# Kernel optimization log

Hardware: AMD Instinct MI355X
Metric: run time of the kernel (lower is better)

The kernel has to match this reference:

```python
import jax, jax.numpy as jnp
import numpy as np

N = 100000   # num_nodes
E = 1250000  # num_edges
IN = 64
HID = 64
OUT = 64
LN_EPS = 1e-5


def _gcn_conv(x, src, dst, W, b, n):
    # PyG GCNConv: add self-loops, symmetric deg^{-1/2} normalization, then linear.
    h = x @ W  # (N, out)
    deg = jax.ops.segment_sum(jnp.ones(src.shape[0], h.dtype), dst, num_segments=n) + 1.0  # +1 self-loop
    dinv = jax.lax.rsqrt(deg)
    norm = dinv[src] * dinv[dst]  # (E,)
    out = jax.ops.segment_sum(h[src] * norm[:, None], dst, num_segments=n)
    out = out + h * (dinv * dinv)[:, None]  # self-loop message
    return out + b


def _sage_conv(x, src, dst, Wl, bl, Wr, n):
    # PyG SAGEConv(aggr='mean'): lin_l(mean_{j in N(i)} x_j) + lin_r(x_i); bias only in lin_l.
    cnt = jax.ops.segment_sum(jnp.ones(src.shape[0], x.dtype), dst, num_segments=n)
    agg = jax.ops.segment_sum(x[src], dst, num_segments=n) / jnp.maximum(cnt, 1.0)[:, None]
    return agg @ Wl + bl + x @ Wr


def _layer_norm(x, g, b):
    mu = jnp.mean(x, axis=-1, keepdims=True)
    var = jnp.var(x, axis=-1, keepdims=True)
    return (x - mu) * jax.lax.rsqrt(var + LN_EPS) * g + b


def setup_inputs() -> dict:
    key = jax.random.key(0)
    ks = jax.random.split(key, 16)
    def w(k, shape):
        fan_in = shape[0]
        return (jax.random.normal(k, shape, jnp.float32) / np.sqrt(fan_in)).astype(jnp.float32)
    x = jax.random.normal(ks[0], (N, IN), jnp.float32)
    edge_index = jax.random.randint(ks[1], (2, E), 0, N, dtype=jnp.int64)
    return {
        "x": x,
        "edge_index": edge_index,
        "gcn_w1": w(ks[2], (IN, HID)), "gcn_b1": jnp.zeros((HID,), jnp.float32),
        "gcn_w2": w(ks[3], (HID, OUT)), "gcn_b2": jnp.zeros((OUT,), jnp.float32),
        "sage_wl1": w(ks[4], (IN, HID)), "sage_bl1": jnp.zeros((HID,), jnp.float32),
        "sage_wr1": w(ks[5], (IN, HID)),
        "sage_wl2": w(ks[6], (HID, OUT)), "sage_bl2": jnp.zeros((OUT,), jnp.float32),
        "sage_wr2": w(ks[7], (HID, OUT)),
        "gcn_ln_g": jnp.ones((OUT,), jnp.float32), "gcn_ln_b": jnp.zeros((OUT,), jnp.float32),
        "sage_ln_g": jnp.ones((OUT,), jnp.float32), "sage_ln_b": jnp.zeros((OUT,), jnp.float32),
        "proj_w": w(ks[8], (2 * OUT, OUT)), "proj_b": jnp.zeros((OUT,), jnp.float32),
    }


def reference(x, edge_index, gcn_w1, gcn_b1, gcn_w2, gcn_b2,
              sage_wl1, sage_bl1, sage_wr1, sage_wl2, sage_bl2, sage_wr2,
              gcn_ln_g, gcn_ln_b, sage_ln_g, sage_ln_b, proj_w, proj_b):
    src, dst = edge_index[0], edge_index[1]
    n = x.shape[0]
    # GCN branch (dropout p=0 / eval -> identity)
    g = jax.nn.relu(_gcn_conv(x, src, dst, gcn_w1, gcn_b1, n))
    g = _gcn_conv(g, src, dst, gcn_w2, gcn_b2, n)
    # SAGE branch
    s = jax.nn.relu(_sage_conv(x, src, dst, sage_wl1, sage_bl1, sage_wr1, n))
    s = _sage_conv(s, src, dst, sage_wl2, sage_bl2, sage_wr2, n)
    # Norm + projected-concat fusion
    g = _layer_norm(g, gcn_ln_g, gcn_ln_b)
    s = _layer_norm(s, sage_ln_g, sage_ln_b)
    cat = jnp.concatenate([g, s], axis=-1)  # (N, 2*OUT)
    return cat @ proj_w + proj_b
```

## Files before the change

### kernel.cpp

```cpp
#include <hip/hip_runtime.h>


#define SCAN_CHUNK 2048

typedef __attribute__((ext_vector_type(8))) short short8;
typedef __attribute__((ext_vector_type(4))) short short4v;
typedef __attribute__((ext_vector_type(4))) float floatx4;

__device__ __forceinline__ unsigned short f2bf(float f) {
    unsigned int u = __float_as_uint(f);
    unsigned int r = u + 0x7FFFu + ((u >> 16) & 1u);
    return (unsigned short)(r >> 16);
}
__device__ __forceinline__ float bf2f(unsigned short h) {
    return __uint_as_float(((unsigned int)h) << 16);
}

__device__ __forceinline__ unsigned lds_addr(const void* p) {
    return (unsigned)(unsigned long long)(__attribute__((address_space(3))) const char*)p;
}

__device__ __forceinline__ void gload_lds16(const void* g, void* l) {
    __builtin_amdgcn_global_load_lds(
        (const __attribute__((address_space(1))) unsigned int*)g,
        (__attribute__((address_space(3))) unsigned int*)l, 16, 0, 0);
}

template<int NN>
__device__ __forceinline__ void wait_vmcnt() {
    if constexpr (NN == 8)      asm volatile("s_waitcnt vmcnt(8)" ::: "memory");
    else if constexpr (NN == 4) asm volatile("s_waitcnt vmcnt(4)" ::: "memory");
    else                        asm volatile("s_waitcnt vmcnt(0)" ::: "memory");
}

__device__ __forceinline__ short8 cat44(short4v lo, short4v hi) {
    short8 r;
    r[0] = lo[0]; r[1] = lo[1]; r[2] = lo[2]; r[3] = lo[3];
    r[4] = hi[0]; r[5] = hi[1]; r[6] = hi[2]; r[7] = hi[3];
    return r;
}

template<int NF, int CTB>
__device__ __forceinline__ void tr_read4(unsigned a0, short8 bf[4]) {
    short4v l0, h0, l1, h1, l2, h2, l3, h3;
    asm volatile(
        "ds_read_b64_tr_b16 %0, %8 offset:%9\n\t"
        "ds_read_b64_tr_b16 %1, %8 offset:%10\n\t"
        "ds_read_b64_tr_b16 %2, %8 offset:%11\n\t"
        "ds_read_b64_tr_b16 %3, %8 offset:%12\n\t"
        "ds_read_b64_tr_b16 %4, %8 offset:%13\n\t"
        "ds_read_b64_tr_b16 %5, %8 offset:%14\n\t"
        "ds_read_b64_tr_b16 %6, %8 offset:%15\n\t"
        "ds_read_b64_tr_b16 %7, %8 offset:%16\n\t"
        "s_waitcnt lgkmcnt(0)"
        : "=&v"(l0), "=&v"(h0), "=&v"(l1), "=&v"(h1),
          "=&v"(l2), "=&v"(h2), "=&v"(l3), "=&v"(h3)
        : "v"(a0),
          "i"((0 * NF + CTB + 0) * 128), "i"((1 * NF + CTB + 0) * 128),
          "i"((0 * NF + CTB + 1) * 128), "i"((1 * NF + CTB + 1) * 128),
          "i"((0 * NF + CTB + 2) * 128), "i"((1 * NF + CTB + 2) * 128),
          "i"((0 * NF + CTB + 3) * 128), "i"((1 * NF + CTB + 3) * 128)
        : "memory");
    bf[0] = cat44(l0, h0);
    bf[1] = cat44(l1, h1);
    bf[2] = cat44(l2, h2);
    bf[3] = cat44(l3, h3);
}

__global__ void k_count(const int* __restrict__ ei, int E, int* __restrict__ cnt,
                        int* __restrict__ rank) {
    int i = blockIdx.x * blockDim.x + threadIdx.x;
    int e = i * 4;
    if (e + 4 <= E) {
        int4 d = *(const int4*)&ei[E + e];
        int4 r;
        r.x = atomicAdd(&cnt[d.x], 1);
        r.y = atomicAdd(&cnt[d.y], 1);
        r.z = atomicAdd(&cnt[d.z], 1);
        r.w = atomicAdd(&cnt[d.w], 1);
        *(int4*)&rank[e] = r;
    } else {
        for (int j = e; j < E; ++j) rank[j] = atomicAdd(&cnt[ei[E + j]], 1);
    }
}

__global__ void k_scan_reduce(const int* __restrict__ cnt, int N, int* __restrict__ blockSums) {
    __shared__ int lds[256];
    int base = blockIdx.x * SCAN_CHUNK;
    int t = threadIdx.x;
    int s = 0;
    for (int j = 0; j < 8; ++j) {
        int idx = base + t * 8 + j;
        if (idx < N) s += cnt[idx] + 1;
    }
    lds[t] = s;
    __syncthreads();
    for (int d = 128; d > 0; d >>= 1) {
        if (t < d) lds[t] += lds[t + d];
        __syncthreads();
    }
    if (t == 0) blockSums[blockIdx.x] = lds[0];
}

__global__ void k_scan_spine(int* __restrict__ blockSums, int B) {
    if (threadIdx.x == 0 && blockIdx.x == 0) {
        int run = 0;
        for (int b = 0; b < B; ++b) { int v = blockSums[b]; blockSums[b] = run; run += v; }
    }
}

__global__ void k_scan_write(const int* __restrict__ cnt, int N,
                             const int* __restrict__ blockSums,
                             int* __restrict__ offs, float* __restrict__ dinv) {
    __shared__ int lds[256];
    int base = blockIdx.x * SCAN_CHUNK;
    int t = threadIdx.x;
    int v[8];
    int s = 0;
    for (int j = 0; j < 8; ++j) {
        int idx = base + t * 8 + j;
        v[j] = (idx < N) ? cnt[idx] : 0;
        s += (idx < N) ? v[j] + 1 : 0;
    }
    lds[t] = s;
    __syncthreads();
    for (int d = 1; d < 256; d <<= 1) {
        int x = (t >= d) ? lds[t - d] : 0;
        __syncthreads();
        lds[t] += x;
        __syncthreads();
    }
    int excl = (t == 0) ? 0 : lds[t - 1];
    int run = blockSums[blockIdx.x] + excl;
    for (int j = 0; j < 8; ++j) {
        int idx = base + t * 8 + j;
        if (idx < N) {
            offs[idx] = run;
            run += v[j] + 1;
            dinv[idx] = rsqrtf((float)v[j] + 1.0f);
            if (idx == N - 1) offs[N] = run;
        }
    }
}

__global__ void k_fill(const int* __restrict__ ei, int E, const int* __restrict__ offs,
                       const int* __restrict__ rank, const float* __restrict__ dinv,
                       int* __restrict__ csr, unsigned int* __restrict__ pk, int use_pk) {
    int i = blockIdx.x * blockDim.x + threadIdx.x;
    int e = i * 4;
    if (e + 4 <= E) {
        int4 s = *(const int4*)&ei[e];
        int4 d = *(const int4*)&ei[E + e];
        int4 r = *(const int4*)&rank[e];
        int p0 = offs[d.x] + r.x, p1 = offs[d.y] + r.y;
        int p2 = offs[d.z] + r.z, p3 = offs[d.w] + r.w;
        csr[p0] = s.x; csr[p1] = s.y; csr[p2] = s.z; csr[p3] = s.w;
        if (use_pk) {
            pk[p0] = ((unsigned)(d.x & 15) << 16) | f2bf(dinv[s.x] * dinv[d.x]);
            pk[p1] = ((unsigned)(d.y & 15) << 16) | f2bf(dinv[s.y] * dinv[d.y]);
            pk[p2] = ((unsigned)(d.z & 15) << 16) | f2bf(dinv[s.z] * dinv[d.z]);
            pk[p3] = ((unsigned)(d.w & 15) << 16) | f2bf(dinv[s.w] * dinv[d.w]);
        }
    } else {
        for (int j = e; j < E; ++j) {
            int dd = ei[E + j];
            int p = offs[dd] + rank[j];
            csr[p] = ei[j];
            if (use_pk) pk[p] = ((unsigned)(dd & 15) << 16) | f2bf(dinv[ei[j]] * dinv[dd]);
        }
    }
}

__global__ void k_self(const int* __restrict__ offs, const int* __restrict__ cnt,
                       const float* __restrict__ dinv,
                       int* __restrict__ csr, unsigned int* __restrict__ pk, int N) {
    int i = blockIdx.x * blockDim.x + threadIdx.x;
    if (i < N) {
        int pos = offs[i] + cnt[i];
        float di = dinv[i];
        csr[pos] = i;
        pk[pos] = ((unsigned)(i & 15) << 16) | (1u << 20) | f2bf(di * di);
    }
}

__global__ void k_xtobf16(const float* __restrict__ x, unsigned short* __restrict__ xb, int total) {
    int i = blockIdx.x * blockDim.x + threadIdx.x;
    int e = i * 8;
    if (e + 8 <= total) {
        float4 a = *(const float4*)&x[e];
        float4 b = *(const float4*)&x[e + 4];
        short8 o;
        o[0] = (short)f2bf(a.x); o[1] = (short)f2bf(a.y);
        o[2] = (short)f2bf(a.z); o[3] = (short)f2bf(a.w);
        o[4] = (short)f2bf(b.x); o[5] = (short)f2bf(b.y);
        o[6] = (short)f2bf(b.z); o[7] = (short)f2bf(b.w);
        *(short8*)&xb[e] = o;
    } else {
        for (int j = e; j < total; ++j) xb[j] = f2bf(x[j]);
    }
}

template<int ROWSH>
__launch_bounds__(128)
__global__ void k_gatherM(const unsigned short* __restrict__ feat,
                          const int* __restrict__ csr,
                          const unsigned int* __restrict__ pk,
                          const int* __restrict__ offs, const int* __restrict__ cnt,
                          unsigned short* __restrict__ agg, int N) {
    constexpr int NF = ROWSH / 16;
    constexpr int LPR = ROWSH / 8;
    constexpr int EPP = 64 / LPR;
    constexpr int PASSES = 32 / EPP;

    __shared__ unsigned short sbuf[2][2][32 * ROWSH];

    const int lane = threadIdx.x & 63;
    const int wv = threadIdx.x >> 6;
    const int base = blockIdx.x * 32 + wv * 16;
    if (base >= N) return;

    const int q = lane >> 4;
    const int d16 = lane & 15;

    const int parity = lane & 1;
    const int ei_low = (lane >> 1) & 3;
    const int sf_sub = (lane >> 3) & (NF - 1);
    const int ei_high = (NF == 8) ? 0 : (lane >> 5);
    const int eid = ei_high * 4 + ei_low;
    const int sf = sf_sub * 16 + parity * 8;

    const int elo = offs[base];
    const int ehi = offs[min(base + 16, N)];
    const int emax = ehi - 1;
    const int nch = (ehi - elo + 31) >> 5;

    int cM0, cM1, cM2, cM3;
    unsigned pM0, pM1, pM2, pM3;
    {
        int i0 = elo + lane;
        int i1 = i0 + 64, i2 = i0 + 128, i3 = i0 + 192;
        cM0 = csr[i0 <= emax ? i0 : emax];
        cM1 = csr[i1 <= emax ? i1 : emax];
        cM2 = csr[i2 <= emax ? i2 : emax];
        cM3 = csr[i3 <= emax ? i3 : emax];
        unsigned t0 = pk[i0 <= emax ? i0 : emax];
        unsigned t1 = pk[i1 <= emax ? i1 : emax];
        unsigned t2 = pk[i2 <= emax ? i2 : emax];
        unsigned t3 = pk[i3 <= emax ? i3 : emax];
        pM0 = (i0 < ehi) ? t0 : 0x00100000u;
        pM1 = (i1 < ehi) ? t1 : 0x00100000u;
        pM2 = (i2 < ehi) ? t2 : 0x00100000u;
        pM3 = (i3 < ehi) ? t3 : 0x00100000u;
    }

    floatx4 accg[4], accs[4];
#pragma unroll
    for (int i = 0; i < 4; ++i) {
        accg[i] = floatx4{0.f, 0.f, 0.f, 0.f};
        accs[i] = floatx4{0.f, 0.f, 0.f, 0.f};
    }

    unsigned short* wb0 = &sbuf[wv][0][0];
    unsigned short* wb1 = &sbuf[wv][1][0];
    const unsigned a0base = (unsigned)(q * 2 * NF) * 128u + (unsigned)d16 * 8u;
    const unsigned a0_0 = lds_addr(wb0) + a0base;
    const unsigned a0_1 = lds_addr(wb1) + a0base;

    auto getmeta = [&](int c, int& cv, unsigned& pv, int& wofs) {
        int rc = c >> 1;
        if (rc < 4) {
            wofs = (c & 1) << 5;
            cv = (rc == 0) ? cM0 : (rc == 1) ? cM1 : (rc == 2) ? cM2 : cM3;
            pv = (rc == 0) ? pM0 : (rc == 1) ? pM1 : (rc == 2) ? pM2 : pM3;
        } else {
            int idx = elo + (c << 5) + lane;
            int idc = idx <= emax ? idx : emax;
            cv = csr[idc];
            unsigned t = pk[idc];
            pv = (idx < ehi) ? t : 0x00100000u;
            wofs = 0;
        }
    };

    auto issue = [&](unsigned short* dst, int cv, int wofs) {
#pragma unroll
        for (int p = 0; p < PASSES; ++p) {
            int src = __shfl(cv, wofs + p * EPP + eid, 64);
            gload_lds16(&feat[(size_t)src * ROWSH + sf], dst + p * 512);
        }
        __builtin_amdgcn_sched_barrier(0);
    };

    int cv; unsigned pv; int wofs;
    getmeta(0, cv, pv, wofs);
    issue(wb0, cv, wofs);
    unsigned pvC = pv; int wofsC = wofs;

    int cur = 0;
    for (int c = 0; c < nch; ++c) {
        bool pf = (c + 1 < nch);
        if (pf) {
            getmeta(c + 1, cv, pv, wofs);
            issue(cur ? wb0 : wb1, cv, wofs);
        }
        short8 aG, aS;
#pragma unroll
        for (int j = 0; j < 8; ++j) {
            unsigned u = (unsigned)__shfl((int)pvC, wofsC + q * 8 + j, 64);
            unsigned hi = u >> 16;
            bool match = (int)(hi & 15u) == d16;
            aG[j] = match ? (short)(u & 0xFFFFu) : (short)0;
            aS[j] = (match && !(hi & 16u)) ? (short)0x3F80 : (short)0;
        }
        if (pf) wait_vmcnt<PASSES>();
        else    wait_vmcnt<0>();
        __builtin_amdgcn_sched_barrier(0);

        const unsigned a0 = cur ? a0_1 : a0_0;
        short8 bG[4];
        tr_read4<NF, 0>(a0, bG);
#pragma unroll
        for (int ct = 0; ct < 4; ++ct)
            accg[ct] = __builtin_amdgcn_mfma_f32_16x16x32_bf16(aG, bG[ct], accg[ct], 0, 0, 0);
        if constexpr (NF == 8) {
            short8 bS[4];
            tr_read4<NF, 4>(a0, bS);
#pragma unroll
            for (int ct = 0; ct < 4; ++ct)
                accs[ct] = __builtin_amdgcn_mfma_f32_16x16x32_bf16(aS, bS[ct], accs[ct], 0, 0, 0);
        } else {
#pragma unroll
            for (int ct = 0; ct < 4; ++ct)
                accs[ct] = __builtin_amdgcn_mfma_f32_16x16x32_bf16(aS, bG[ct], accs[ct], 0, 0, 0);
        }
        pvC = pv; wofsC = wofs;
        cur ^= 1;
    }

#pragma unroll
    for (int r = 0; r < 4; ++r) {
        int node = base + q * 4 + r;
        if (node < N) {
            float rn = 1.0f / fmaxf((float)cnt[node], 1.0f);
#pragma unroll
            for (int ct = 0; ct < 4; ++ct) {
                agg[(size_t)node * 128 + ct * 16 + d16]      = f2bf(accg[ct][r]);
                agg[(size_t)node * 128 + 64 + ct * 16 + d16] = f2bf(accs[ct][r] * rn);
            }
        }
    }
}

__device__ __forceinline__ void xor_reduce8(float4& a, float4& b) {
    a.x += __shfl_xor(a.x, 16, 64); a.y += __shfl_xor(a.y, 16, 64);
    a.z += __shfl_xor(a.z, 16, 64); a.w += __shfl_xor(a.w, 16, 64);
    b.x += __shfl_xor(b.x, 16, 64); b.y += __shfl_xor(b.y, 16, 64);
    b.z += __shfl_xor(b.z, 16, 64); b.w += __shfl_xor(b.w, 16, 64);
    a.x += __shfl_xor(a.x, 32, 64); a.y += __shfl_xor(a.y, 32, 64);
    a.z += __shfl_xor(a.z, 32, 64); a.w += __shfl_xor(a.w, 32, 64);
    b.x += __shfl_xor(b.x, 32, 64); b.y += __shfl_xor(b.y, 32, 64);
    b.z += __shfl_xor(b.z, 32, 64); b.w += __shfl_xor(b.w, 32, 64);
}

__device__ __forceinline__ float red16(float v) {
    v += __shfl_xor(v, 1, 64);
    v += __shfl_xor(v, 2, 64);
    v += __shfl_xor(v, 4, 64);
    v += __shfl_xor(v, 8, 64);
    return v;
}

__global__ void k_gather1_f32(const float* __restrict__ x, const int* __restrict__ csr,
                              const int* __restrict__ offs, const int* __restrict__ cnt,
                              const float* __restrict__ dinv,
                              unsigned short* __restrict__ agg, int N) {
    int lane = threadIdx.x & 63;
    int wave = threadIdx.x >> 6;
    int node = blockIdx.x * 4 + wave;
    if (node >= N) return;
    int c = lane & 15, grp = lane >> 4;

    int st = offs[node];
    int cn = cnt[node];
    float di = dinv[node];

    float4 aA = {0.f, 0.f, 0.f, 0.f}, aB = {0.f, 0.f, 0.f, 0.f};
    for (int e = 0; e < cn; e += 8) {
        int i0 = e + grp, i1 = e + 4 + grp;
        float m0 = (i0 < cn) ? 1.f : 0.f;
        float m1 = (i1 < cn) ? 1.f : 0.f;
        int s0 = csr[st + (i0 < cn ? i0 : cn - 1)];
        int s1 = csr[st + (i1 < cn ? i1 : cn - 1)];
        float w0 = m0 * dinv[s0];
        float w1 = m1 * dinv[s1];
        float4 v0 = *(const float4*)&x[(size_t)s0 * 64 + 4 * c];
        float4 v1 = *(const float4*)&x[(size_t)s1 * 64 + 4 * c];
        aA.x += w0 * v0.x + w1 * v1.x; aA.y += w0 * v0.y + w1 * v1.y;
        aA.z += w0 * v0.z + w1 * v1.z; aA.w += w0 * v0.w + w1 * v1.w;
        aB.x += m0 * v0.x + m1 * v1.x; aB.y += m0 * v0.y + m1 * v1.y;
        aB.z += m0 * v0.z + m1 * v1.z; aB.w += m0 * v0.w + m1 * v1.w;
    }
    xor_reduce8(aA, aB);

    if (grp == 0) {
        float4 sq = *(const float4*)&x[(size_t)node * 64 + 4 * c];
        float d2 = di * di;
        ushort4 o;
        o.x = f2bf(di * aA.x + d2 * sq.x); o.y = f2bf(di * aA.y + d2 * sq.y);
        o.z = f2bf(di * aA.z + d2 * sq.z); o.w = f2bf(di * aA.w + d2 * sq.w);
        *(ushort4*)&agg[(size_t)node * 128 + 4 * c] = o;
    } else if (grp == 1) {
        float rn = 1.0f / fmaxf((float)cn, 1.0f);
        ushort4 o;
        o.x = f2bf(aB.x * rn); o.y = f2bf(aB.y * rn);
        o.z = f2bf(aB.z * rn); o.w = f2bf(aB.w * rn);
        *(ushort4*)&agg[(size_t)node * 128 + 64 + 4 * c] = o;
    }
}

__global__ void k_gather2(const unsigned short* __restrict__ gs, const int* __restrict__ csr,
                          const int* __restrict__ offs, const int* __restrict__ cnt,
                          const float* __restrict__ dinv,
                          unsigned short* __restrict__ agg, int N) {
    int lane = threadIdx.x & 63;
    int wave = threadIdx.x >> 6;
    int node = blockIdx.x * 4 + wave;
    if (node >= N) return;
    int c = lane & 15, grp = lane >> 4;

    int st = offs[node];
    int cn = cnt[node];
    float di = dinv[node];

    float4 aC = {0.f, 0.f, 0.f, 0.f}, aD = {0.f, 0.f, 0.f, 0.f};
    for (int e = 0; e < cn; e += 8) {
        int i0 = e + grp, i1 = e + 4 + grp;
        float m0 = (i0 < cn) ? 1.f : 0.f;
        float m1 = (i1 < cn) ? 1.f : 0.f;
        int s0 = csr[st + (i0 < cn ? i0 : cn - 1)];
        int s1 = csr[st + (i1 < cn ? i1 : cn - 1)];
        float w0 = m0 * dinv[s0];
        float w1 = m1 * dinv[s1];
        const unsigned short* p0 = gs + (size_t)s0 * 128 + 4 * c;
        const unsigned short* p1 = gs + (size_t)s1 * 128 + 4 * c;
        ushort4 g0u = *(const ushort4*)p0;
        ushort4 g1u = *(const ushort4*)p1;
        ushort4 t0u = *(const ushort4*)(p0 + 64);
        ushort4 t1u = *(const ushort4*)(p1 + 64);
        aC.x += w0 * bf2f(g0u.x) + w1 * bf2f(g1u.x);
        aC.y += w0 * bf2f(g0u.y) + w1 * bf2f(g1u.y);
        aC.z += w0 * bf2f(g0u.z) + w1 * bf2f(g1u.z);
        aC.w += w0 * bf2f(g0u.w) + w1 * bf2f(g1u.w);
        aD.x += m0 * bf2f(t0u.x) + m1 * bf2f(t1u.x);
        aD.y += m0 * bf2f(t0u.y) + m1 * bf2f(t1u.y);
        aD.z += m0 * bf2f(t0u.z) + m1 * bf2f(t1u.z);
        aD.w += m0 * bf2f(t0u.w) + m1 * bf2f(t1u.w);
    }
    xor_reduce8(aC, aD);

    if (grp == 0) {
        ushort4 su = *(const ushort4*)&gs[(size_t)node * 128 + 4 * c];
        float d2 = di * di;
        ushort4 o;
        o.x = f2bf(di * aC.x + d2 * bf2f(su.x));
        o.y = f2bf(di * aC.y + d2 * bf2f(su.y));
        o.z = f2bf(di * aC.z + d2 * bf2f(su.z));
        o.w = f2bf(di * aC.w + d2 * bf2f(su.w));
        *(ushort4*)&agg[(size_t)node * 128 + 4 * c] = o;
    } else if (grp == 1) {
        float rn = 1.0f / fmaxf((float)cn, 1.0f);
        ushort4 o;
        o.x = f2bf(aD.x * rn); o.y = f2bf(aD.y * rn);
        o.z = f2bf(aD.z * rn); o.w = f2bf(aD.w * rn);
        *(ushort4*)&agg[(size_t)node * 128 + 64 + 4 * c] = o;
    }
}

__launch_bounds__(512, 1)
__global__ void k_gemm1(const unsigned short* __restrict__ agg,
                        const unsigned short* __restrict__ xb,
                        const float* __restrict__ xf, int use_xb,
                        const float* __restrict__ W1, const float* __restrict__ b1,
                        const float* __restrict__ Wl1, const float* __restrict__ bl1,
                        const float* __restrict__ Wr1,
                        unsigned short* __restrict__ buf1, int N) {
    alignas(16) __shared__ unsigned short sW[3][4096];
    int t = threadIdx.x;
    for (int i = t; i < 1536; i += 512) {
        int m = i >> 9;
        int rem = i & 511;
        int f = rem >> 6;
        int L = rem & 63;
        int kb = (f >> 2) * 32 + (L >> 4) * 8;
        int o = (f & 3) * 16 + (L & 15);
        const float* Wsrc = (m == 0) ? W1 : (m == 1) ? Wl1 : Wr1;
        unsigned short* dst = &sW[m][f * 512 + L * 8];
        #pragma unroll
        for (int j = 0; j < 8; ++j) dst[j] = f2bf(Wsrc[(kb + j) * 64 + o]);
    }
    __syncthreads();

    int lane = t & 63;
    int wave = t >> 6;
    int quad = lane >> 4;
    int n16 = lane & 15;
    int base = blockIdx.x * 128 + wave * 16;
    if (base >= N) return;

    int nm = base + n16;
    if (nm >= N) nm = N - 1;
    const unsigned short* ar = agg + (size_t)nm * 128;

    {
        short8 a0 = *(const short8*)(ar + quad * 8);
        short8 a1 = *(const short8*)(ar + 32 + quad * 8);
        floatx4 g0 = {0.f, 0.f, 0.f, 0.f}, g1 = g0, g2 = g0, g3 = g0;
        g0 = __builtin_amdgcn_mfma_f32_16x16x32_bf16(a0, *(const short8*)&sW[0][0 * 512 + lane * 8], g0, 0, 0, 0);
        g0 = __builtin_amdgcn_mfma_f32_16x16x32_bf16(a1, *(const short8*)&sW[0][4 * 512 + lane * 8], g0, 0, 0, 0);
        g1 = __builtin_amdgcn_mfma_f32_16x16x32_bf16(a0, *(const short8*)&sW[0][1 * 512 + lane * 8], g1, 0, 0, 0);
        g1 = __builtin_amdgcn_mfma_f32_16x16x32_bf16(a1, *(const short8*)&sW[0][5 * 512 + lane * 8], g1, 0, 0, 0);
        g2 = __builtin_amdgcn_mfma_f32_16x16x32_bf16(a0, *(const short8*)&sW[0][2 * 512 + lane * 8], g2, 0, 0, 0);
        g2 = __builtin_amdgcn_mfma_f32_16x16x32_bf16(a1, *(const short8*)&sW[0][6 * 512 + lane * 8], g2, 0, 0, 0);
        g3 = __builtin_amdgcn_mfma_f32_16x16x32_bf16(a0, *(const short8*)&sW[0][3 * 512 + lane * 8], g3, 0, 0, 0);
        g3 = __builtin_amdgcn_mfma_f32_16x16x32_bf16(a1, *(const short8*)&sW[0][7 * 512 + lane * 8], g3, 0, 0, 0);
        floatx4 gt[4] = {g0, g1, g2, g3};
        #pragma unroll
        for (int nt = 0; nt < 4; ++nt) {
            float bg = b1[nt * 16 + n16];
            #pragma unroll
            for (int r = 0; r < 4; ++r) {
                int node = base + quad * 4 + r;
                if (node < N)
                    buf1[(size_t)node * 128 + nt * 16 + n16] = f2bf(fmaxf(gt[nt][r] + bg, 0.f));
            }
        }
    }

    {
        short8 a0 = *(const short8*)(ar + 64 + quad * 8);
        short8 a1 = *(const short8*)(ar + 96 + quad * 8);
        short8 ax0, ax1;
        if (use_xb) {
            ax0 = *(const short8*)&xb[(size_t)nm * 64 + quad * 8];
            ax1 = *(const short8*)&xb[(size_t)nm * 64 + 32 + quad * 8];
        } else {
            float4 xq0 = *(const float4*)&xf[(size_t)nm * 64 + quad * 8];
            float4 xq1 = *(const float4*)&xf[(size_t)nm * 64 + quad * 8 + 4];
            float4 xq2 = *(const float4*)&xf[(size_t)nm * 64 + 32 + quad * 8];
            float4 xq3 = *(const float4*)&xf[(size_t)nm * 64 + 32 + quad * 8 + 4];
            ax0[0] = (short)f2bf(xq0.x); ax0[1] = (short)f2bf(xq0.y);
            ax0[2] = (short)f2bf(xq0.z); ax0[3] = (short)f2bf(xq0.w);
            ax0[4] = (short)f2bf(xq1.x); ax0[5] = (short)f2bf(xq1.y);
            ax0[6] = (short)f2bf(xq1.z); ax0[7] = (short)f2bf(xq1.w);
            ax1[0] = (short)f2bf(xq2.x); ax1[1] = (short)f2bf(xq2.y);
            ax1[2] = (short)f2bf(xq2.z); ax1[3] = (short)f2bf(xq2.w);
            ax1[4] = (short)f2bf(xq3.x); ax1[5] = (short)f2bf(xq3.y);
            ax1[6] = (short)f2bf(xq3.z); ax1[7] = (short)f2bf(xq3.w);
        }

        floatx4 s0 = {0.f, 0.f, 0.f, 0.f}, s1 = s0, s2 = s0, s3 = s0;
        s0 = __builtin_amdgcn_mfma_f32_16x16x32_bf16(a0, *(const short8*)&sW[1][0 * 512 + lane * 8], s0, 0, 0, 0);
        s0 = __builtin_amdgcn_mfma_f32_16x16x32_bf16(a1, *(const short8*)&sW[1][4 * 512 + lane * 8], s0, 0, 0, 0);
        s0 = __builtin_amdgcn_mfma_f32_16x16x32_bf16(ax0, *(const short8*)&sW[2][0 * 512 + lane * 8], s0, 0, 0, 0);
        s0 = __builtin_amdgcn_mfma_f32_16x16x32_bf16(ax1, *(const short8*)&sW[2][4 * 512 + lane * 8], s0, 0, 0, 0);
        s1 = __builtin_amdgcn_mfma_f32_16x16x32_bf16(a0, *(const short8*)&sW[1][1 * 512 + lane * 8], s1, 0, 0, 0);
        s1 = __builtin_amdgcn_mfma_f32_16x16x32_bf16(a1, *(const short8*)&sW[1][5 * 512 + lane * 8], s1, 0, 0, 0);
        s1 = __builtin_amdgcn_mfma_f32_16x16x32_bf16(ax0, *(const short8*)&sW[2][1 * 512 + lane * 8], s1, 0, 0, 0);
        s1 = __builtin_amdgcn_mfma_f32_16x16x32_bf16(ax1, *(const short8*)&sW[2][5 * 512 + lane * 8], s1, 0, 0, 0);
        s2 = __builtin_amdgcn_mfma_f32_16x16x32_bf16(a0, *(const short8*)&sW[1][2 * 512 + lane * 8], s2, 0, 0, 0);
        s2 = __builtin_amdgcn_mfma_f32_16x16x32_bf16(a1, *(const short8*)&sW[1][6 * 512 + lane * 8], s2, 0, 0, 0);
        s2 = __builtin_amdgcn_mfma_f32_16x16x32_bf16(ax0, *(const short8*)&sW[2][2 * 512 + lane * 8], s2, 0, 0, 0);
        s2 = __builtin_amdgcn_mfma_f32_16x16x32_bf16(ax1, *(const short8*)&sW[2][6 * 512 + lane * 8], s2, 0, 0, 0);
        s3 = __builtin_amdgcn_mfma_f32_16x16x32_bf16(a0, *(const short8*)&sW[1][3 * 512 + lane * 8], s3, 0, 0, 0);
        s3 = __builtin_amdgcn_mfma_f32_16x16x32_bf16(a1, *(const short8*)&sW[1][7 * 512 + lane * 8], s3, 0, 0, 0);
        s3 = __builtin_amdgcn_mfma_f32_16x16x32_bf16(ax0, *(const short8*)&sW[2][3 * 512 + lane * 8], s3, 0, 0, 0);
        s3 = __builtin_amdgcn_mfma_f32_16x16x32_bf16(ax1, *(const short8*)&sW[2][7 * 512 + lane * 8], s3, 0, 0, 0);
        floatx4 stl[4] = {s0, s1, s2, s3};
        #pragma unroll
        for (int nt = 0; nt < 4; ++nt) {
            float bs = bl1[nt * 16 + n16];
            #pragma unroll
            for (int r = 0; r < 4; ++r) {
                int node = base + quad * 4 + r;
                if (node < N)
                    buf1[(size_t)node * 128 + 64 + nt * 16 + n16] = f2bf(fmaxf(stl[nt][r] + bs, 0.f));
            }
        }
    }
}

__launch_bounds__(512, 1)
__global__ void k_gemm2(const unsigned short* __restrict__ agg,
                        const unsigned short* __restrict__ buf1,
                        const float* __restrict__ W2, const float* __restrict__ b2,
                        const float* __restrict__ Wl2, const float* __restrict__ bl2,
                        const float* __restrict__ Wr2,
                        const float* __restrict__ lngG, const float* __restrict__ lnbG,
                        const float* __restrict__ lngS, const float* __restrict__ lnbS,
                        const float* __restrict__ Pw, const float* __restrict__ Pb,
                        float* __restrict__ out, int N) {
    alignas(16) __shared__ unsigned short sW[3][4096];
    alignas(16) __shared__ unsigned short sP[8192];
    alignas(16) __shared__ unsigned short sT[8][16 * 132];
    int t = threadIdx.x;
    for (int i = t; i < 1536; i += 512) {
        int m = i >> 9;
        int rem = i & 511;
        int f = rem >> 6;
        int L = rem & 63;
        int kb = (f >> 2) * 32 + (L >> 4) * 8;
        int o = (f & 3) * 16 + (L & 15);
        const float* Wsrc = (m == 0) ? W2 : (m == 1) ? Wl2 : Wr2;
        unsigned short* dst = &sW[m][f * 512 + L * 8];
        #pragma unroll
        for (int j = 0; j < 8; ++j) dst[j] = f2bf(Wsrc[(kb + j) * 64 + o]);
    }
    for (int i = t; i < 1024; i += 512) {
        int f = i >> 6;
        int L = i & 63;
        int kb = (f >> 2) * 32 + (L >> 4) * 8;
        int o = (f & 3) * 16 + (L & 15);
        unsigned short* dst = &sP[f * 512 + L * 8];
        #pragma unroll
        for (int j = 0; j < 8; ++j) dst[j] = f2bf(Pw[(kb + j) * 64 + o]);
    }
    __syncthreads();

    int lane = t & 63;
    int wave = t >> 6;
    int quad = lane >> 4;
    int n16 = lane & 15;
    int base = blockIdx.x * 128 + wave * 16;
    if (base >= N) return;
    int nm = base + n16;
    if (nm >= N) nm = N - 1;
    const unsigned short* ar = agg + (size_t)nm * 128;
    const unsigned short* br = buf1 + (size_t)nm * 128;
    unsigned short* tw = &sT[wave][0];

    {
        short8 a0 = *(const short8*)(ar + quad * 8);
        short8 a1 = *(const short8*)(ar + 32 + quad * 8);
        floatx4 c0 = {0.f, 0.f, 0.f, 0.f}, c1 = c0, c2 = c0, c3 = c0;
        c0 = __builtin_amdgcn_mfma_f32_16x16x32_bf16(a0, *(const short8*)&sW[0][0 * 512 + lane * 8], c0, 0, 0, 0);
        c0 = __builtin_amdgcn_mfma_f32_16x16x32_bf16(a1, *(const short8*)&sW[0][4 * 512 + lane * 8], c0, 0, 0, 0);
        c1 = __builtin_amdgcn_mfma_f32_16x16x32_bf16(a0, *(const short8*)&sW[0][1 * 512 + lane * 8], c1, 0, 0, 0);
        c1 = __builtin_amdgcn_mfma_f32_16x16x32_bf16(a1, *(const short8*)&sW[0][5 * 512 + lane * 8], c1, 0, 0, 0);
        c2 = __builtin_amdgcn_mfma_f32_16x16x32_bf16(a0, *(const short8*)&sW[0][2 * 512 + lane * 8], c2, 0, 0, 0);
        c2 = __builtin_amdgcn_mfma_f32_16x16x32_bf16(a1, *(const short8*)&sW[0][6 * 512 + lane * 8], c2, 0, 0, 0);
        c3 = __builtin_amdgcn_mfma_f32_16x16x32_bf16(a0, *(const short8*)&sW[0][3 * 512 + lane * 8], c3, 0, 0, 0);
        c3 = __builtin_amdgcn_mfma_f32_16x16x32_bf16(a1, *(const short8*)&sW[0][7 * 512 + lane * 8], c3, 0, 0, 0);

        float bv0 = b2[n16], bv1 = b2[16 + n16], bv2 = b2[32 + n16], bv3 = b2[48 + n16];
        float gv0 = lngG[n16], gv1 = lngG[16 + n16], gv2 = lngG[32 + n16], gv3 = lngG[48 + n16];
        float ev0 = lnbG[n16], ev1 = lnbG[16 + n16], ev2 = lnbG[32 + n16], ev3 = lnbG[48 + n16];
        #pragma unroll
        for (int r = 0; r < 4; ++r) {
            float z0 = c0[r] + bv0, z1 = c1[r] + bv1, z2 = c2[r] + bv2, z3 = c3[r] + bv3;
            float s = red16(z0 + z1 + z2 + z3);
            float q = red16(z0 * z0 + z1 * z1 + z2 * z2 + z3 * z3);
            float mu = s * (1.0f / 64.0f);
            float var = fmaxf(q * (1.0f / 64.0f) - mu * mu, 0.0f);
            float rs = rsqrtf(var + 1e-5f);
            unsigned short* row = tw + (quad * 4 + r) * 132;
            row[n16]      = f2bf((z0 - mu) * rs * gv0 + ev0);
            row[16 + n16] = f2bf((z1 - mu) * rs * gv1 + ev1);
            row[32 + n16] = f2bf((z2 - mu) * rs * gv2 + ev2);
            row[48 + n16] = f2bf((z3 - mu) * rs * gv3 + ev3);
        }
    }

    {
        short8 a0 = *(const short8*)(ar + 64 + quad * 8);
        short8 a1 = *(const short8*)(ar + 96 + quad * 8);
        short8 v0 = *(const short8*)(br + 64 + quad * 8);
        short8 v1 = *(const short8*)(br + 96 + quad * 8);
        floatx4 c0 = {0.f, 0.f, 0.f, 0.f}, c1 = c0, c2 = c0, c3 = c0;
        c0 = __builtin_amdgcn_mfma_f32_16x16x32_bf16(a0, *(const short8*)&sW[1][0 * 512 + lane * 8], c0, 0, 0, 0);
        c0 = __builtin_amdgcn_mfma_f32_16x16x32_bf16(a1, *(const short8*)&sW[1][4 * 512 + lane * 8], c0, 0, 0, 0);
        c0 = __builtin_amdgcn_mfma_f32_16x16x32_bf16(v0, *(const short8*)&sW[2][0 * 512 + lane * 8], c0, 0, 0, 0);
        c0 = __builtin_amdgcn_mfma_f32_16x16x32_bf16(v1, *(const short8*)&sW[2][4 * 512 + lane * 8], c0, 0, 0, 0);
        c1 = __builtin_amdgcn_mfma_f32_16x16x32_bf16(a0, *(const short8*)&sW[1][1 * 512 + lane * 8], c1, 0, 0, 0);
        c1 = __builtin_amdgcn_mfma_f32_16x16x32_bf16(a1, *(const short8*)&sW[1][5 * 512 + lane * 8], c1, 0, 0, 0);
        c1 = __builtin_amdgcn_mfma_f32_16x16x32_bf16(v0, *(const short8*)&sW[2][1 * 512 + lane * 8], c1, 0, 0, 0);
        c1 = __builtin_amdgcn_mfma_f32_16x16x32_bf16(v1, *(const short8*)&sW[2][5 * 512 + lane * 8], c1, 0, 0, 0);
        c2 = __builtin_amdgcn_mfma_f32_16x16x32_bf16(a0, *(const short8*)&sW[1][2 * 512 + lane * 8], c2, 0, 0, 0);
        c2 = __builtin_amdgcn_mfma_f32_16x16x32_bf16(a1, *(const short8*)&sW[1][6 * 512 + lane * 8], c2, 0, 0, 0);
        c2 = __builtin_amdgcn_mfma_f32_16x16x32_bf16(v0, *(const short8*)&sW[2][2 * 512 + lane * 8], c2, 0, 0, 0);
        c2 = __builtin_amdgcn_mfma_f32_16x16x32_bf16(v1, *(const short8*)&sW[2][6 * 512 + lane * 8], c2, 0, 0, 0);
        c3 = __builtin_amdgcn_mfma_f32_16x16x32_bf16(a0, *(const short8*)&sW[1][3 * 512 + lane * 8], c3, 0, 0, 0);
        c3 = __builtin_amdgcn_mfma_f32_16x16x32_bf16(a1, *(const short8*)&sW[1][7 * 512 + lane * 8], c3, 0, 0, 0);
        c3 = __builtin_amdgcn_mfma_f32_16x16x32_bf16(v0, *(const short8*)&sW[2][3 * 512 + lane * 8], c3, 0, 0, 0);
        c3 = __builtin_amdgcn_mfma_f32_16x16x32_bf16(v1, *(const short8*)&sW[2][7 * 512 + lane * 8], c3, 0, 0, 0);

        float bv0 = bl2[n16], bv1 = bl2[16 + n16], bv2 = bl2[32 + n16], bv3 = bl2[48 + n16];
        float gv0 = lngS[n16], gv1 = lngS[16 + n16], gv2 = lngS[32 + n16], gv3 = lngS[48 + n16];
        float ev0 = lnbS[n16], ev1 = lnbS[16 + n16], ev2 = lnbS[32 + n16], ev3 = lnbS[48 + n16];
        #pragma unroll
        for (int r = 0; r < 4; ++r) {
            float z0 = c0[r] + bv0, z1 = c1[r] + bv1, z2 = c2[r] + bv2, z3 = c3[r] + bv3;
            float s = red16(z0 + z1 + z2 + z3);
            float q = red16(z0 * z0 + z1 * z1 + z2 * z2 + z3 * z3);
            float mu = s * (1.0f / 64.0f);
            float var = fmaxf(q * (1.0f / 64.0f) - mu * mu, 0.0f);
            float rs = rsqrtf(var + 1e-5f);
            unsigned short* row = tw + (quad * 4 + r) * 132 + 64;
            row[n16]      = f2bf((z0 - mu) * rs * gv0 + ev0);
            row[16 + n16] = f2bf((z1 - mu) * rs * gv1 + ev1);
            row[32 + n16] = f2bf((z2 - mu) * rs * gv2 + ev2);
            row[48 + n16] = f2bf((z3 - mu) * rs * gv3 + ev3);
        }
    }

    floatx4 o0 = {0.f, 0.f, 0.f, 0.f}, o1 = o0, o2 = o0, o3 = o0;
    #pragma unroll
    for (int ks = 0; ks < 4; ++ks) {
        const unsigned short* ap = tw + n16 * 132 + ks * 32 + quad * 8;
        short4v lo = *(const short4v*)ap;
        short4v hi = *(const short4v*)(ap + 4);
        short8 af;
        af[0] = lo[0]; af[1] = lo[1]; af[2] = lo[2]; af[3] = lo[3];
        af[4] = hi[0]; af[5] = hi[1]; af[6] = hi[2]; af[7] = hi[3];
        o0 = __builtin_amdgcn_mfma_f32_16x16x32_bf16(af, *(const short8*)&sP[(ks * 4 + 0) * 512 + lane * 8], o0, 0, 0, 0);
        o1 = __builtin_amdgcn_mfma_f32_16x16x32_bf16(af, *(const short8*)&sP[(ks * 4 + 1) * 512 + lane * 8], o1, 0, 0, 0);
        o2 = __builtin_amdgcn_mfma_f32_16x16x32_bf16(af, *(const short8*)&sP[(ks * 4 + 2) * 512 + lane * 8], o2, 0, 0, 0);
        o3 = __builtin_amdgcn_mfma_f32_16x16x32_bf16(af, *(const short8*)&sP[(ks * 4 + 3) * 512 + lane * 8], o3, 0, 0, 0);
    }
    float p0 = Pb[n16], p1 = Pb[16 + n16], p2 = Pb[32 + n16], p3 = Pb[48 + n16];
    floatx4 ot[4] = {o0, o1, o2, o3};
    float pv[4] = {p0, p1, p2, p3};
    #pragma unroll
    for (int nt = 0; nt < 4; ++nt) {
        #pragma unroll
        for (int r = 0; r < 4; ++r) {
            int node = base + quad * 4 + r;
            if (node < N) out[(size_t)node * 64 + nt * 16 + n16] = ot[nt][r] + pv[nt];
        }
    }
}

extern "C" void kernel_launch(void* const* d_in, const int* in_sizes, int n_in,
                              void* d_out, int out_size, void* d_ws, size_t ws_size,
                              hipStream_t stream) {
    const float* x        = (const float*)d_in[0];
    const int*   ei       = (const int*)d_in[1];
    const float* gcn_w1   = (const float*)d_in[2];
    const float* gcn_b1   = (const float*)d_in[3];
    const float* gcn_w2   = (const float*)d_in[4];
    const float* gcn_b2   = (const float*)d_in[5];
    const float* sage_wl1 = (const float*)d_in[6];
    const float* sage_bl1 = (const float*)d_in[7];
    const float* sage_wr1 = (const float*)d_in[8];
    const float* sage_wl2 = (const float*)d_in[9];
    const float* sage_bl2 = (const float*)d_in[10];
    const float* sage_wr2 = (const float*)d_in[11];
    const float* gcn_ln_g = (const float*)d_in[12];
    const float* gcn_ln_b = (const float*)d_in[13];
    const float* sage_ln_g = (const float*)d_in[14];
    const float* sage_ln_b = (const float*)d_in[15];
    const float* proj_w   = (const float*)d_in[16];
    const float* proj_b   = (const float*)d_in[17];
    float* out = (float*)d_out;

    const int N = in_sizes[0] / 64;
    const int E = in_sizes[1] / 2;
    const int B = (N + SCAN_CHUNK - 1) / SCAN_CHUNK;

    char* w = (char*)d_ws;
    size_t off = 0;
    auto alloc = [&](size_t bytes) -> void* {
        void* p = w + off;
        off = (off + bytes + 255) & ~(size_t)255;
        return p;
    };
    int*            cnt       = (int*)alloc((size_t)N * 4);
    int*            offs      = (int*)alloc((size_t)(N + 1) * 4);
    float*          dinv      = (float*)alloc((size_t)N * 4);
    int*            blockSums = (int*)alloc((size_t)(B + 1) * 4);
    int*            csr       = (int*)alloc((size_t)(E + N + 64) * 4);
    unsigned short* agg       = (unsigned short*)alloc((size_t)N * 128 * 2);
    unsigned short* buf1      = (unsigned short*)alloc((size_t)N * 128 * 2);
    size_t off_nonew = off;
    unsigned int*   pk        = (unsigned int*)alloc((size_t)(E + N + 64) * 4);
    unsigned short* xb        = (unsigned short*)alloc((size_t)N * 64 * 2);
    int use_new = (off <= ws_size) ? 1 : 0;
    if (!use_new) off = off_nonew;
    int* rank = (int*)agg;
    (void)n_in; (void)out_size;

    hipMemsetAsync(cnt, 0, (size_t)N * 4, stream);

    int e4Blocks = ((E + 3) / 4 + 255) / 256;
    k_count<<<e4Blocks, 256, 0, stream>>>(ei, E, cnt, rank);
    k_scan_reduce<<<B, 256, 0, stream>>>(cnt, N, blockSums);
    k_scan_spine<<<1, 64, 0, stream>>>(blockSums, B);
    k_scan_write<<<B, 256, 0, stream>>>(cnt, N, blockSums, offs, dinv);
    k_fill<<<e4Blocks, 256, 0, stream>>>(ei, E, offs, rank, dinv, csr, pk, use_new);

    if (use_new) {
        k_self<<<(N + 255) / 256, 256, 0, stream>>>(offs, cnt, dinv, csr, pk, N);
        int xBlocks = ((N * 64 + 7) / 8 + 255) / 256;
        k_xtobf16<<<xBlocks, 256, 0, stream>>>(x, xb, N * 64);
        k_gatherM<64><<<(N + 31) / 32, 128, 0, stream>>>(xb, csr, pk, offs, cnt, agg, N);
        k_gemm1<<<(N + 127) / 128, 512, 0, stream>>>(agg, xb, x, 1, gcn_w1, gcn_b1,
                                                     sage_wl1, sage_bl1, sage_wr1, buf1, N);
        k_gatherM<128><<<(N + 31) / 32, 128, 0, stream>>>(buf1, csr, pk, offs, cnt, agg, N);
    } else {
        k_gather1_f32<<<(N + 3) / 4, 256, 0, stream>>>(x, csr, offs, cnt, dinv, agg, N);
        k_gemm1<<<(N + 127) / 128, 512, 0, stream>>>(agg, xb, x, 0, gcn_w1, gcn_b1,
                                                     sage_wl1, sage_bl1, sage_wr1, buf1, N);
        k_gather2<<<(N + 3) / 4, 256, 0, stream>>>(buf1, csr, offs, cnt, dinv, agg, N);
    }
    k_gemm2<<<(N + 127) / 128, 512, 0, stream>>>(agg, buf1, gcn_w2, gcn_b2,
                                                 sage_wl2, sage_bl2, sage_wr2,
                                                 gcn_ln_g, gcn_ln_b, sage_ln_g, sage_ln_b,
                                                 proj_w, proj_b, out, N);
}
```

Before: 361.8 us.

## Fuse x-to-bf16 into count and self-loops into fill; simplify gather staging

Folds the bf16 conversion of x into the edge-count kernel and the self-loop CSR entries into the fill kernel, removing two launches. The gather kernel drops its double-buffered async global-to-LDS loads and instead loads through registers, then stores to a single LDS buffer. It also doubles the block size to four waves covering 64 nodes. This trades load/compute overlap in the gather for lower LDS use and higher occupancy. The fused kernels may also be imbalanced, since the count grid now has to cover both the edges and the feature elements.

Result: faster. 334.4 us (-7.6%).

```diff
diff --git a/kernel.cpp b/kernel.cpp
--- a/kernel.cpp
+++ b/kernel.cpp
@@ -18,19 +18,6 @@
 
 __device__ __forceinline__ unsigned lds_addr(const void* p) {
     return (unsigned)(unsigned long long)(__attribute__((address_space(3))) const char*)p;
-}
-
-__device__ __forceinline__ void gload_lds16(const void* g, void* l) {
-    __builtin_amdgcn_global_load_lds(
-        (const __attribute__((address_space(1))) unsigned int*)g,
-        (__attribute__((address_space(3))) unsigned int*)l, 16, 0, 0);
-}
-
-template<int NN>
-__device__ __forceinline__ void wait_vmcnt() {
-    if constexpr (NN == 8)      asm volatile("s_waitcnt vmcnt(8)" ::: "memory");
-    else if constexpr (NN == 4) asm volatile("s_waitcnt vmcnt(4)" ::: "memory");
-    else                        asm volatile("s_waitcnt vmcnt(0)" ::: "memory");
 }
 
 __device__ __forceinline__ short8 cat44(short4v lo, short4v hi) {
@@ -68,7 +55,9 @@
 }
 
 __global__ void k_count(const int* __restrict__ ei, int E, int* __restrict__ cnt,
-                        int* __restrict__ rank) {
+                        int* __restrict__ rank,
+                        const float* __restrict__ x, unsigned short* __restrict__ xb,
+                        int xtotal, int do_x) {
     int i = blockIdx.x * blockDim.x + threadIdx.x;
     int e = i * 4;
     if (e + 4 <= E) {
@@ -79,8 +68,23 @@
         r.z = atomicAdd(&cnt[d.z], 1);
         r.w = atomicAdd(&cnt[d.w], 1);
         *(int4*)&rank[e] = r;
-    } else {
+    } else if (e < E) {
         for (int j = e; j < E; ++j) rank[j] = atomicAdd(&cnt[ei[E + j]], 1);
+    }
+    if (do_x) {
+        int xe = i * 8;
+        if (xe + 8 <= xtotal) {
+            float4 a = *(const float4*)&x[xe];
+            float4 b = *(const float4*)&x[xe + 4];
+            short8 o;
+            o[0] = (short)f2bf(a.x); o[1] = (short)f2bf(a.y);
+            o[2] = (short)f2bf(a.z); o[3] = (short)f2bf(a.w);
+            o[4] = (short)f2bf(b.x); o[5] = (short)f2bf(b.y);
+            o[6] = (short)f2bf(b.z); o[7] = (short)f2bf(b.w);
+            *(short8*)&xb[xe] = o;
+        } else if (xe < xtotal) {
+            for (int j = xe; j < xtotal; ++j) xb[j] = f2bf(x[j]);
+        }
     }
 }
 
@@ -144,8 +148,10 @@
 }
 
 __global__ void k_fill(const int* __restrict__ ei, int E, const int* __restrict__ offs,
-                       const int* __restrict__ rank, const float* __restrict__ dinv,
-                       int* __restrict__ csr, unsigned int* __restrict__ pk, int use_pk) {
+                       const int* __restrict__ rank, const int* __restrict__ cnt,
+                       const float* __restrict__ dinv,
+                       int* __restrict__ csr, unsigned int* __restrict__ pk,
+                       int use_pk, int N) {
     int i = blockIdx.x * blockDim.x + threadIdx.x;
     int e = i * 4;
     if (e + 4 <= E) {
@@ -161,7 +167,7 @@
             pk[p2] = ((unsigned)(d.z & 15) << 16) | f2bf(dinv[s.z] * dinv[d.z]);
             pk[p3] = ((unsigned)(d.w & 15) << 16) | f2bf(dinv[s.w] * dinv[d.w]);
         }
-    } else {
+    } else if (e < E) {
         for (int j = e; j < E; ++j) {
             int dd = ei[E + j];
             int p = offs[dd] + rank[j];
@@ -169,13 +175,7 @@
             if (use_pk) pk[p] = ((unsigned)(dd & 15) << 16) | f2bf(dinv[ei[j]] * dinv[dd]);
         }
     }
-}
-
-__global__ void k_self(const int* __restrict__ offs, const int* __restrict__ cnt,
-                       const float* __restrict__ dinv,
-                       int* __restrict__ csr, unsigned int* __restrict__ pk, int N) {
-    int i = blockIdx.x * blockDim.x + threadIdx.x;
-    if (i < N) {
+    if (use_pk && i < N) {
         int pos = offs[i] + cnt[i];
         float di = dinv[i];
         csr[pos] = i;
@@ -183,25 +183,8 @@
     }
 }
 
-__global__ void k_xtobf16(const float* __restrict__ x, unsigned short* __restrict__ xb, int total) {
-    int i = blockIdx.x * blockDim.x + threadIdx.x;
-    int e = i * 8;
-    if (e + 8 <= total) {
-        float4 a = *(const float4*)&x[e];
-        float4 b = *(const float4*)&x[e + 4];
-        short8 o;
-        o[0] = (short)f2bf(a.x); o[1] = (short)f2bf(a.y);
-        o[2] = (short)f2bf(a.z); o[3] = (short)f2bf(a.w);
-        o[4] = (short)f2bf(b.x); o[5] = (short)f2bf(b.y);
-        o[6] = (short)f2bf(b.z); o[7] = (short)f2bf(b.w);
-        *(short8*)&xb[e] = o;
-    } else {
-        for (int j = e; j < total; ++j) xb[j] = f2bf(x[j]);
-    }
-}
-
 template<int ROWSH>
-__launch_bounds__(128)
+__launch_bounds__(256)
 __global__ void k_gatherM(const unsigned short* __restrict__ feat,
                           const int* __restrict__ csr,
                           const unsigned int* __restrict__ pk,
@@ -212,11 +195,11 @@
     constexpr int EPP = 64 / LPR;
     constexpr int PASSES = 32 / EPP;
 
-    __shared__ unsigned short sbuf[2][2][32 * ROWSH];
+    __shared__ unsigned short sbuf[4][32 * ROWSH];
 
     const int lane = threadIdx.x & 63;
     const int wv = threadIdx.x >> 6;
-    const int base = blockIdx.x * 32 + wv * 16;
+    const int base = blockIdx.x * 64 + wv * 16;
     if (base >= N) return;
 
     const int q = lane >> 4;
@@ -260,13 +243,11 @@
         accs[i] = floatx4{0.f, 0.f, 0.f, 0.f};
     }
 
-    unsigned short* wb0 = &sbuf[wv][0][0];
-    unsigned short* wb1 = &sbuf[wv][1][0];
-    const unsigned a0base = (unsigned)(q * 2 * NF) * 128u + (unsigned)d16 * 8u;
-    const unsigned a0_0 = lds_addr(wb0) + a0base;
-    const unsigned a0_1 = lds_addr(wb1) + a0base;
-
-    auto getmeta = [&](int c, int& cv, unsigned& pv, int& wofs) {
+    unsigned short* wb = &sbuf[wv][0];
+    const unsigned a0 = lds_addr(wb) + (unsigned)(q * 2 * NF) * 128u + (unsigned)d16 * 8u;
+
+    for (int c = 0; c < nch; ++c) {
+        int cv; unsigned pv; int wofs;
         int rc = c >> 1;
         if (rc < 4) {
             wofs = (c & 1) << 5;
@@ -280,43 +261,30 @@
             pv = (idx < ehi) ? t : 0x00100000u;
             wofs = 0;
         }
-    };
-
-    auto issue = [&](unsigned short* dst, int cv, int wofs) {
+
+        short8 stg[PASSES];
 #pragma unroll
         for (int p = 0; p < PASSES; ++p) {
             int src = __shfl(cv, wofs + p * EPP + eid, 64);
-            gload_lds16(&feat[(size_t)src * ROWSH + sf], dst + p * 512);
-        }
-        __builtin_amdgcn_sched_barrier(0);
-    };
-
-    int cv; unsigned pv; int wofs;
-    getmeta(0, cv, pv, wofs);
-    issue(wb0, cv, wofs);
-    unsigned pvC = pv; int wofsC = wofs;
-
-    int cur = 0;
-    for (int c = 0; c < nch; ++c) {
-        bool pf = (c + 1 < nch);
-        if (pf) {
-            getmeta(c + 1, cv, pv, wofs);
-            issue(cur ? wb0 : wb1, cv, wofs);
-        }
+            stg[p] = *(const short8*)&feat[(size_t)src * ROWSH + sf];
+        }
+
         short8 aG, aS;
 #pragma unroll
         for (int j = 0; j < 8; ++j) {
-            unsigned u = (unsigned)__shfl((int)pvC, wofsC + q * 8 + j, 64);
+            unsigned u = (unsigned)__shfl((int)pv, wofs + q * 8 + j, 64);
             unsigned hi = u >> 16;
             bool match = (int)(hi & 15u) == d16;
             aG[j] = match ? (short)(u & 0xFFFFu) : (short)0;
             aS[j] = (match && !(hi & 16u)) ? (short)0x3F80 : (short)0;
         }
-        if (pf) wait_vmcnt<PASSES>();
-        else    wait_vmcnt<0>();
+
+#pragma unroll
+        for (int p = 0; p < PASSES; ++p)
+            *(short8*)&wb[p * 512 + lane * 8] = stg[p];
+        asm volatile("s_waitcnt lgkmcnt(0)" ::: "memory");
         __builtin_amdgcn_sched_barrier(0);
 
-        const unsigned a0 = cur ? a0_1 : a0_0;
         short8 bG[4];
         tr_read4<NF, 0>(a0, bG);
 #pragma unroll
@@ -333,8 +301,6 @@
             for (int ct = 0; ct < 4; ++ct)
                 accs[ct] = __builtin_amdgcn_mfma_f32_16x16x32_bf16(aS, bG[ct], accs[ct], 0, 0, 0);
         }
-        pvC = pv; wofsC = wofs;
-        cur ^= 1;
     }
 
 #pragma unroll
@@ -791,20 +757,19 @@
     hipMemsetAsync(cnt, 0, (size_t)N * 4, stream);
 
     int e4Blocks = ((E + 3) / 4 + 255) / 256;
-    k_count<<<e4Blocks, 256, 0, stream>>>(ei, E, cnt, rank);
+    int x8Blocks = ((N * 64 + 7) / 8 + 255) / 256;
+    int cntBlocks = use_new ? max(e4Blocks, x8Blocks) : e4Blocks;
+    k_count<<<cntBlocks, 256, 0, stream>>>(ei, E, cnt, rank, x, xb, N * 64, use_new);
     k_scan_reduce<<<B, 256, 0, stream>>>(cnt, N, blockSums);
     k_scan_spine<<<1, 64, 0, stream>>>(blockSums, B);
     k_scan_write<<<B, 256, 0, stream>>>(cnt, N, blockSums, offs, dinv);
-    k_fill<<<e4Blocks, 256, 0, stream>>>(ei, E, offs, rank, dinv, csr, pk, use_new);
+    k_fill<<<e4Blocks, 256, 0, stream>>>(ei, E, offs, rank, cnt, dinv, csr, pk, use_new, N);
 
     if (use_new) {
-        k_self<<<(N + 255) / 256, 256, 0, stream>>>(offs, cnt, dinv, csr, pk, N);
-        int xBlocks = ((N * 64 + 7) / 8 + 255) / 256;
-        k_xtobf16<<<xBlocks, 256, 0, stream>>>(x, xb, N * 64);
-        k_gatherM<64><<<(N + 31) / 32, 128, 0, stream>>>(xb, csr, pk, offs, cnt, agg, N);
+        k_gatherM<64><<<(N + 63) / 64, 256, 0, stream>>>(xb, csr, pk, offs, cnt, agg, N);
         k_gemm1<<<(N + 127) / 128, 512, 0, stream>>>(agg, xb, x, 1, gcn_w1, gcn_b1,
                                                      sage_wl1, sage_bl1, sage_wr1, buf1, N);
-        k_gatherM<128><<<(N + 31) / 32, 128, 0, stream>>>(buf1, csr, pk, offs, cnt, agg, N);
+        k_gatherM<128><<<(N + 63) / 64, 256, 0, stream>>>(buf1, csr, pk, offs, cnt, agg, N);
     } else {
         k_gather1_f32<<<(N + 3) / 4, 256, 0, stream>>>(x, csr, offs, cnt, dinv, agg, N);
         k_gemm1<<<(N + 127) / 128, 512, 0, stream>>>(agg, xb, x, 0, gcn_w1, gcn_b1,
```
